# Performance work log

Hardware: AMD Instinct MI355X
Metric: run time of the kernel (lower is better)

Reference implementation:

```python
import jax, jax.numpy as jnp
import numpy as np

B, L, D_MODEL = 2, 2048, 1024
N_HEAD, D_K, D_V = 16, 64, 64


def setup_inputs() -> dict:
    key = jax.random.key(0)
    ks = jax.random.split(key, 11)
    s = lambda fan_in: 1.0 / np.sqrt(fan_in)
    return {
        "q": jax.random.normal(ks[0], (B, L, D_MODEL), dtype=jnp.float32),
        "k": jax.random.normal(ks[1], (B, L, D_MODEL), dtype=jnp.float32),
        "v": jax.random.normal(ks[2], (B, L, D_MODEL), dtype=jnp.float32),
        "Wq": jax.random.uniform(ks[3], (D_MODEL, N_HEAD * D_K), jnp.float32, -s(D_MODEL), s(D_MODEL)),
        "bq": jax.random.uniform(ks[4], (N_HEAD * D_K,), jnp.float32, -s(D_MODEL), s(D_MODEL)),
        "Wk": jax.random.uniform(ks[5], (D_MODEL, N_HEAD * D_K), jnp.float32, -s(D_MODEL), s(D_MODEL)),
        "bk": jax.random.uniform(ks[6], (N_HEAD * D_K,), jnp.float32, -s(D_MODEL), s(D_MODEL)),
        "Wv": jax.random.uniform(ks[7], (D_MODEL, N_HEAD * D_V), jnp.float32, -s(D_MODEL), s(D_MODEL)),
        "bv": jax.random.uniform(ks[8], (N_HEAD * D_V,), jnp.float32, -s(D_MODEL), s(D_MODEL)),
        "Wo": jax.random.uniform(ks[9], (N_HEAD * D_V, D_MODEL), jnp.float32, -s(N_HEAD * D_V), s(N_HEAD * D_V)),
        "bo": jax.random.uniform(ks[10], (D_MODEL,), jnp.float32, -s(N_HEAD * D_V), s(N_HEAD * D_V)),
    }


def reference(q, k, v, Wq, bq, Wk, bk, Wv, bv, Wo, bo):
    b, lq, _ = q.shape
    lk = k.shape[1]
    # QKV projections then split heads: [B, H, L, Dk]
    qh = (q @ Wq + bq).reshape(b, lq, N_HEAD, D_K).transpose(0, 2, 1, 3)
    kh = (k @ Wk + bk).reshape(b, lk, N_HEAD, D_K).transpose(0, 2, 1, 3)
    vh = (v @ Wv + bv).reshape(b, lk, N_HEAD, D_V).transpose(0, 2, 1, 3)
    # naive SDPA: materialize [B, H, Lq, Lk] scores, scale by sqrt(d_k)
    scores = jnp.einsum("bhqd,bhkd->bhqk", qh, kh) / jnp.sqrt(jnp.float32(D_K))
    attn = jax.nn.softmax(scores, axis=-1)
    out = jnp.einsum("bhqk,bhkd->bhqd", attn, vh)
    # merge heads and output projection (dropout = identity in eval)
    out = out.transpose(0, 2, 1, 3).reshape(b, lq, N_HEAD * D_V)
    out = out @ Wo + bo
    return out, attn
```

## Files before the change

kernel.cpp:

```cpp
#include <hip/hip_runtime.h>
#include <hip/hip_bf16.h>

typedef float f32x4 __attribute__((ext_vector_type(4)));
typedef short bf16x8 __attribute__((ext_vector_type(8)));

#define MFMA_BF16 __builtin_amdgcn_mfma_f32_16x16x32_bf16

static __device__ __forceinline__ unsigned short f2bf(float f) {
    __hip_bfloat16 h = __float2bfloat16(f);
    return __builtin_bit_cast(unsigned short, h);
}
static __device__ __forceinline__ unsigned int pack2(float a, float b) {
    return (unsigned int)f2bf(a) | ((unsigned int)f2bf(b) << 16);
}

static __device__ __forceinline__ void gl16(const unsigned short* g, unsigned short* l) {
    unsigned short* gg = const_cast<unsigned short*>(g);
    __builtin_amdgcn_global_load_lds(
        (__attribute__((address_space(1))) unsigned int*)gg,
        (__attribute__((address_space(3))) unsigned int*)l, 16, 0, 0);
}

__global__ __launch_bounds__(256) void conv_wT(
    const float* __restrict__ Wq, const float* __restrict__ Wk,
    const float* __restrict__ Wv, const float* __restrict__ Wo,
    unsigned short* __restrict__ WT)
{
    const int z = blockIdx.z;
    const float* W = (z == 0) ? Wq : (z == 1) ? Wk : (z == 2) ? Wv : Wo;
    unsigned short* Wt = WT + (size_t)z * 1048576;
    const int k0 = blockIdx.x * 64, n0 = blockIdx.y * 64;
    __shared__ float tl[64][68];
    const int t = threadIdx.x;
    const int r = t >> 2, cs = (t & 3) * 16;
#pragma unroll
    for (int j = 0; j < 4; j++)
        *(float4*)&tl[r][cs + j * 4] = *(const float4*)&W[(size_t)(k0 + r) * 1024 + n0 + cs + j * 4];
    __syncthreads();
    const int n = t & 63, kb = (t >> 6) * 16;
#pragma unroll
    for (int j = 0; j < 4; j++) {
        const int kk = kb + j * 4;
        uint2 o = { pack2(tl[kk][n], tl[kk + 1][n]), pack2(tl[kk + 2][n], tl[kk + 3][n]) };
        *(uint2*)&Wt[(size_t)(n0 + n) * 1024 + k0 + kk] = o;
    }
}

__global__ __launch_bounds__(256) void conv_bf16(
    const float* __restrict__ q, const float* __restrict__ k, const float* __restrict__ v,
    unsigned short* __restrict__ qkvb)
{
    const int z = blockIdx.y;
    const float* s = (z == 0) ? q : (z == 1) ? k : v;
    unsigned short* d = qkvb + (size_t)z * 4194304;
    const size_t i = ((size_t)blockIdx.x * 256 + threadIdx.x) * 8;
    float4 a = *(const float4*)&s[i], b = *(const float4*)&s[i + 4];
    uint4 o = { pack2(a.x, a.y), pack2(a.z, a.w), pack2(b.x, b.y), pack2(b.z, b.w) };
    *(uint4*)&d[i] = o;
}

static __device__ __forceinline__ void gemm_core(
    const unsigned short* __restrict__ A, const unsigned short* __restrict__ Bt,
    unsigned short* lA, unsigned short* lB, int m0, int n0, f32x4 (&acc)[4][4])
{
    const int t = threadIdx.x;
    const int w = t >> 6, lane = t & 63, lrow = lane & 15, lkg = lane >> 4;
    const int wr = w >> 1, wc = w & 1;
    const int srow = lane >> 2, sseg = (lane & 3) * 8;

    const unsigned short* Ab0 = &A[(size_t)(m0 + w * 32 + srow) * 1024 + sseg];
    const unsigned short* Ab1 = &A[(size_t)(m0 + w * 32 + 16 + srow) * 1024 + sseg];
    const unsigned short* Bb0 = &Bt[(size_t)(n0 + w * 32 + srow) * 1024 + sseg];
    const unsigned short* Bb1 = &Bt[(size_t)(n0 + w * 32 + 16 + srow) * 1024 + sseg];

#define GISSUE(tt, buf)                                     \
    do {                                                    \
        const int k0_ = (tt) * 32;                          \
        gl16(Ab0 + k0_, &lA[(buf) * 4096 + w * 1024]);      \
        gl16(Ab1 + k0_, &lA[(buf) * 4096 + w * 1024 + 512]);\
        gl16(Bb0 + k0_, &lB[(buf) * 4096 + w * 1024]);      \
        gl16(Bb1 + k0_, &lB[(buf) * 4096 + w * 1024 + 512]);\
    } while (0)

    GISSUE(0, 0);
    GISSUE(1, 1);
    __builtin_amdgcn_sched_barrier(0);

    int bcur = 0;
    for (int tt = 0; tt < 32; ++tt) {
        if (tt < 31) { asm volatile("s_waitcnt vmcnt(4)"); }
        else         { asm volatile("s_waitcnt vmcnt(0)"); }
        __builtin_amdgcn_s_barrier();
        __builtin_amdgcn_sched_barrier(0);
        if (tt + 2 < 32) {
            int bpre = bcur + 2; if (bpre >= 3) bpre -= 3;
            GISSUE(tt + 2, bpre);
        }
        __builtin_amdgcn_sched_barrier(0);

        const unsigned short* la = &lA[bcur * 4096];
        const unsigned short* lb = &lB[bcur * 4096];
        bf16x8 af[4], bfr[4];
#pragma unroll
        for (int mi = 0; mi < 4; mi++)
            af[mi] = *(const bf16x8*)&la[(wr * 64 + mi * 16 + lrow) * 32 + lkg * 8];
#pragma unroll
        for (int ni = 0; ni < 4; ni++)
            bfr[ni] = *(const bf16x8*)&lb[(wc * 64 + ni * 16 + lrow) * 32 + lkg * 8];
        __builtin_amdgcn_s_setprio(1);
#pragma unroll
        for (int mi = 0; mi < 4; mi++)
#pragma unroll
            for (int ni = 0; ni < 4; ni++)
                acc[mi][ni] = MFMA_BF16(af[mi], bfr[ni], acc[mi][ni], 0, 0, 0);
        __builtin_amdgcn_s_setprio(0);
        bcur = (bcur == 2) ? 0 : bcur + 1;
    }
#undef GISSUE
}

__global__ __launch_bounds__(256) void gemm_qkv(
    const unsigned short* __restrict__ qkvb, const unsigned short* __restrict__ WT,
    const float* __restrict__ bq, const float* __restrict__ bk, const float* __restrict__ bv,
    unsigned short* __restrict__ Qh, unsigned short* __restrict__ Kh, unsigned short* __restrict__ Vt)
{
    const int u0 = blockIdx.x;
    const int u = (u0 & 7) * 96 + (u0 >> 3);
    const int z = u >> 8, rm = u & 255;
    const int m0 = ((rm >> 3) & 31) * 128, n0 = (rm & 7) * 128;

    const unsigned short* A = qkvb + (size_t)z * 4194304;
    const unsigned short* Bt = WT + (size_t)z * 1048576;
    const float* bias = (z == 0) ? bq : (z == 1) ? bk : bv;

    __shared__ unsigned short lA[3 * 4096], lB[3 * 4096];
    f32x4 acc[4][4];
#pragma unroll
    for (int i = 0; i < 4; i++)
#pragma unroll
        for (int j = 0; j < 4; j++) acc[i][j] = (f32x4){0.f, 0.f, 0.f, 0.f};

    gemm_core(A, Bt, lA, lB, m0, n0, acc);

    const int t = threadIdx.x;
    const int w = t >> 6, lane = t & 63, lrow = lane & 15, lkg = lane >> 4;
    const int wr = w >> 1, wc = w & 1;

#pragma unroll
    for (int mi = 0; mi < 4; mi++) {
#pragma unroll
        for (int ni = 0; ni < 4; ni++) {
            const int gn = n0 + wc * 64 + ni * 16 + lrow;
            const float bb = bias[gn];
            const int hh = gn >> 6, dk = gn & 63;
            const int gm0 = m0 + wr * 64 + mi * 16 + lkg * 4;
            const int b2 = gm0 >> 11, ll = gm0 & 2047;
            if (z < 2) {
                unsigned short* C = (z == 0) ? Qh : Kh;
#pragma unroll
                for (int r = 0; r < 4; r++)
                    C[(size_t)((b2 * 16 + hh) * 2048 + ll + r) * 64 + dk] = f2bf(acc[mi][ni][r] + bb);
            } else {
                uint2 o = { pack2(acc[mi][ni][0] + bb, acc[mi][ni][1] + bb),
                            pack2(acc[mi][ni][2] + bb, acc[mi][ni][3] + bb) };
                *(uint2*)&Vt[(size_t)((b2 * 16 + hh) * 64 + dk) * 2048 + ll] = o;
            }
        }
    }
}

__global__ __launch_bounds__(256) void gemm_o(
    const unsigned short* __restrict__ Oh, const unsigned short* __restrict__ WoT,
    const float* __restrict__ bo, float* __restrict__ out)
{
    const int u0 = blockIdx.x;
    const int u = (u0 & 7) * 32 + (u0 >> 3);
    const int m0 = (u >> 3) * 128, n0 = (u & 7) * 128;

    __shared__ unsigned short lA[3 * 4096], lB[3 * 4096];
    f32x4 acc[4][4];
#pragma unroll
    for (int i = 0; i < 4; i++)
#pragma unroll
        for (int j = 0; j < 4; j++) acc[i][j] = (f32x4){0.f, 0.f, 0.f, 0.f};

    gemm_core(Oh, WoT, lA, lB, m0, n0, acc);

    const int t = threadIdx.x;
    const int w = t >> 6, lane = t & 63, lrow = lane & 15, lkg = lane >> 4;
    const int wr = w >> 1, wc = w & 1;

#pragma unroll
    for (int mi = 0; mi < 4; mi++) {
#pragma unroll
        for (int ni = 0; ni < 4; ni++) {
            const int gn = n0 + wc * 64 + ni * 16 + lrow;
            const float bb = bo[gn];
            const int gm0 = m0 + wr * 64 + mi * 16 + lkg * 4;
#pragma unroll
            for (int r = 0; r < 4; r++)
                out[(size_t)(gm0 + r) * 1024 + gn] = acc[mi][ni][r] + bb;
        }
    }
}

__global__ __launch_bounds__(256, 4) void attn_kernel(
    const unsigned short* __restrict__ Qh, const unsigned short* __restrict__ Kh,
    const unsigned short* __restrict__ Vt, float* __restrict__ attn,
    unsigned short* __restrict__ Oh)
{
    const int bid = blockIdx.x;
    const int swz = (bid & 7) * 128 + (bid >> 3);
    const int bh = swz >> 5;
    const int q0 = (swz & 31) * 64;
    const int b = bh >> 4, h = bh & 15;
    const int t = threadIdx.x;
    const int w = t >> 6, lane = t & 63, ql = lane & 15, kg = lane >> 4;

    __shared__ unsigned short regA[8192];
    __shared__ unsigned short kv[8192];

    const size_t kvbase = (size_t)bh * 2048 * 64;
    const float C = 0.18033688011112042f;

    const unsigned short* qptr = Qh + kvbase + (size_t)(q0 + w * 16 + ql) * 64 + kg * 8;
    const bf16x8 qf0 = *(const bf16x8*)(qptr);
    const bf16x8 qf1 = *(const bf16x8*)(qptr + 32);

    const unsigned short* Kbh = Kh + kvbase;
    const unsigned short* Vbh = Vt + kvbase;

    const int kr = w * 16 + (lane >> 3);
    const int kc = (lane & 7) ^ (kr & 7);
    const int r7 = ql & 7;

    f32x4 ls4 = (f32x4){0.f, 0.f, 0.f, 0.f};
    {
        gl16(Kbh + (size_t)kr * 64 + kc * 8, &regA[w * 1024]);
        gl16(Kbh + (size_t)(kr + 8) * 64 + kc * 8, &regA[w * 1024 + 512]);
        __syncthreads();
        for (int kt = 0; kt < 32; ++kt) {
            const int c = kt & 1;
            if (kt < 31) {
                const int k0n = (kt + 1) * 64;
                gl16(Kbh + (size_t)(k0n + kr) * 64 + kc * 8, &regA[(c ^ 1) * 4096 + w * 1024]);
                gl16(Kbh + (size_t)(k0n + kr + 8) * 64 + kc * 8, &regA[(c ^ 1) * 4096 + w * 1024 + 512]);
            } else {
                gl16(Kbh + (size_t)kr * 64 + kc * 8, &kv[w * 1024]);
                gl16(Kbh + (size_t)(kr + 8) * 64 + kc * 8, &kv[w * 1024 + 512]);
                gl16(Vbh + (size_t)kr * 2048 + kc * 8, &kv[4096 + w * 1024]);
                gl16(Vbh + (size_t)(kr + 8) * 2048 + kc * 8, &kv[4096 + w * 1024 + 512]);
            }
            const unsigned short* Kl = &regA[c * 4096];
            f32x4 sacc[4];
            __builtin_amdgcn_s_setprio(1);
#pragma unroll
            for (int ni = 0; ni < 4; ni++) {
                const int rb = (ni * 16 + ql) * 64;
                bf16x8 kf0 = *(const bf16x8*)&Kl[rb + ((kg ^ r7) * 8)];
                bf16x8 kf1 = *(const bf16x8*)&Kl[rb + (((4 + kg) ^ r7) * 8)];
                f32x4 s = (f32x4){0.f, 0.f, 0.f, 0.f};
                s = MFMA_BF16(kf0, qf0, s, 0, 0, 0);
                sacc[ni] = MFMA_BF16(kf1, qf1, s, 0, 0, 0);
            }
            __builtin_amdgcn_s_setprio(0);
#pragma unroll
            for (int ni = 0; ni < 4; ni++)
#pragma unroll
                for (int r = 0; r < 4; r++) ls4[r] += exp2f(sacc[ni][r] * C);
            __syncthreads();
        }
    }
    float lsum = ls4[0] + ls4[1] + ls4[2] + ls4[3];
    lsum += __shfl_xor(lsum, 16);
    lsum += __shfl_xor(lsum, 32);
    const float mlg = -log2f(lsum);

    f32x4 acco[4];
#pragma unroll
    for (int nv = 0; nv < 4; nv++) acco[nv] = (f32x4){0.f, 0.f, 0.f, 0.f};

    float* stgW = (float*)regA + w * 1024;
    const unsigned short* kvK = kv;
    const unsigned short* kvV = kv + 4096;
    float* abase = attn + ((size_t)bh * 2048 + q0 + w * 16) * 2048 + ql * 4;

    for (int kt = 0; kt < 32; ++kt) {
        const int k0 = kt * 64;

        f32x4 sacc[4];
        __builtin_amdgcn_s_setprio(1);
#pragma unroll
        for (int ni = 0; ni < 4; ni++) {
            const int rb = (ni * 16 + ql) * 64;
            bf16x8 kf0 = *(const bf16x8*)&kvK[rb + ((kg ^ r7) * 8)];
            bf16x8 kf1 = *(const bf16x8*)&kvK[rb + (((4 + kg) ^ r7) * 8)];
            f32x4 s = (f32x4){0.f, 0.f, 0.f, 0.f};
            s = MFMA_BF16(kf0, qf0, s, 0, 0, 0);
            sacc[ni] = MFMA_BF16(kf1, qf1, s, 0, 0, 0);
        }
        __builtin_amdgcn_s_setprio(0);

#pragma unroll
        for (int ni = 0; ni < 4; ni++) {
            f32x4 p;
#pragma unroll
            for (int r = 0; r < 4; r++) p[r] = exp2f(fmaf(sacc[ni][r], C, mlg));
            *(f32x4*)&stgW[ql * 64 + ni * 16 + kg * 4] = p;
        }

        __builtin_amdgcn_s_setprio(1);
#pragma unroll
        for (int s4 = 0; s4 < 2; s4++) {
            const float* ps = &stgW[ql * 64 + s4 * 32 + kg * 8];
            f32x4 pa = *(const f32x4*)ps;
            f32x4 pb = *(const f32x4*)(ps + 4);
            uint4 pw = { pack2(pa[0], pa[1]), pack2(pa[2], pa[3]),
                         pack2(pb[0], pb[1]), pack2(pb[2], pb[3]) };
            bf16x8 pf = __builtin_bit_cast(bf16x8, pw);
#pragma unroll
            for (int nv = 0; nv < 4; nv++) {
                const int cc = (s4 * 4 + kg) ^ r7;
                bf16x8 vf = *(const bf16x8*)&kvV[(nv * 16 + ql) * 64 + cc * 8];
                acco[nv] = MFMA_BF16(vf, pf, acco[nv], 0, 0, 0);
            }
        }
        __builtin_amdgcn_s_setprio(0);

        __builtin_amdgcn_s_barrier();
        __builtin_amdgcn_sched_barrier(0);

        if (kt < 31) {
            const int k0n = (kt + 1) * 64;
            gl16(Kbh + (size_t)(k0n + kr) * 64 + kc * 8, &kv[w * 1024]);
            gl16(Kbh + (size_t)(k0n + kr + 8) * 64 + kc * 8, &kv[w * 1024 + 512]);
            gl16(Vbh + (size_t)kr * 2048 + k0n + kc * 8, &kv[4096 + w * 1024]);
            gl16(Vbh + (size_t)(kr + 8) * 2048 + k0n + kc * 8, &kv[4096 + w * 1024 + 512]);
        }
        __builtin_amdgcn_sched_barrier(0);

#pragma unroll
        for (int i = 0; i < 4; i++) {
            const int row = i * 4 + kg;
            f32x4 vv = *(const f32x4*)&stgW[row * 64 + ql * 4];
            __builtin_nontemporal_store(vv, (f32x4*)&abase[(size_t)row * 2048 + k0]);
        }

        asm volatile("s_waitcnt vmcnt(4)");
        __builtin_amdgcn_s_barrier();
        __builtin_amdgcn_sched_barrier(0);
    }
    asm volatile("s_waitcnt vmcnt(0)");

    unsigned short* obase = Oh + ((size_t)(b * 2048 + q0 + w * 16 + ql)) * 1024 + h * 64 + kg * 4;
#pragma unroll
    for (int nv = 0; nv < 4; nv++) {
        uint2 o2 = { pack2(acco[nv][0], acco[nv][1]), pack2(acco[nv][2], acco[nv][3]) };
        *(uint2*)&obase[nv * 16] = o2;
    }
}

extern "C" void kernel_launch(void* const* d_in, const int* in_sizes, int n_in,
                              void* d_out, int out_size, void* d_ws, size_t ws_size,
                              hipStream_t stream) {
    const float* q  = (const float*)d_in[0];
    const float* k  = (const float*)d_in[1];
    const float* v  = (const float*)d_in[2];
    const float* Wq = (const float*)d_in[3];
    const float* bq = (const float*)d_in[4];
    const float* Wk = (const float*)d_in[5];
    const float* bk = (const float*)d_in[6];
    const float* Wv = (const float*)d_in[7];
    const float* bv = (const float*)d_in[8];
    const float* Wo = (const float*)d_in[9];
    const float* bo = (const float*)d_in[10];

    float* out  = (float*)d_out;
    float* attn = out + (size_t)2 * 2048 * 1024;

    const size_t HS = 4194304;
    unsigned short* qkvb = (unsigned short*)d_ws;
    unsigned short* WT   = qkvb + 3 * HS;
    unsigned short* Qh   = WT + 4 * 1048576;
    unsigned short* Kh   = Qh + HS;
    unsigned short* Vt   = Kh + HS;
    unsigned short* Oh   = Vt + HS;

    conv_wT  <<<dim3(16, 16, 4), 256, 0, stream>>>(Wq, Wk, Wv, Wo, WT);
    conv_bf16<<<dim3(2048, 3),  256, 0, stream>>>(q, k, v, qkvb);
    gemm_qkv <<<dim3(768), 256, 0, stream>>>(qkvb, WT, bq, bk, bv, Qh, Kh, Vt);
    attn_kernel<<<dim3(1024), 256, 0, stream>>>(Qh, Kh, Vt, attn, Oh);
    gemm_o   <<<dim3(256), 256, 0, stream>>>(Oh, WT + 3 * 1048576, bo, out);
}
```

Measured before the change: 242.2 us.

## Vectorize GEMM epilogue stores via swapped MFMA operands and LDS-staged V transpose

```diff
diff --git a/kernel.cpp b/kernel.cpp
--- a/kernel.cpp
+++ b/kernel.cpp
@@ -37,12 +37,16 @@
     for (int j = 0; j < 4; j++)
         *(float4*)&tl[r][cs + j * 4] = *(const float4*)&W[(size_t)(k0 + r) * 1024 + n0 + cs + j * 4];
     __syncthreads();
-    const int n = t & 63, kb = (t >> 6) * 16;
-#pragma unroll
-    for (int j = 0; j < 4; j++) {
-        const int kk = kb + j * 4;
-        uint2 o = { pack2(tl[kk][n], tl[kk + 1][n]), pack2(tl[kk + 2][n], tl[kk + 3][n]) };
-        *(uint2*)&Wt[(size_t)(n0 + n) * 1024 + k0 + kk] = o;
+#pragma unroll
+    for (int pass = 0; pass < 2; pass++) {
+        const int n = (t >> 3) + pass * 32;
+        const int ks = (t & 7) * 8;
+        uint4 o;
+        unsigned int* op = (unsigned int*)&o;
+#pragma unroll
+        for (int j = 0; j < 4; j++)
+            op[j] = pack2(tl[ks + 2 * j][n], tl[ks + 2 * j + 1][n]);
+        *(uint4*)&Wt[(size_t)(n0 + n) * 1024 + k0 + ks] = o;
     }
 }
 
@@ -59,6 +63,7 @@
     *(uint4*)&d[i] = o;
 }
 
+template <bool SWAP>
 static __device__ __forceinline__ void gemm_core(
     const unsigned short* __restrict__ A, const unsigned short* __restrict__ Bt,
     unsigned short* lA, unsigned short* lB, int m0, int n0, f32x4 (&acc)[4][4])
@@ -111,27 +116,30 @@
 #pragma unroll
         for (int mi = 0; mi < 4; mi++)
 #pragma unroll
-            for (int ni = 0; ni < 4; ni++)
-                acc[mi][ni] = MFMA_BF16(af[mi], bfr[ni], acc[mi][ni], 0, 0, 0);
+            for (int ni = 0; ni < 4; ni++) {
+                if (SWAP) acc[mi][ni] = MFMA_BF16(bfr[ni], af[mi], acc[mi][ni], 0, 0, 0);
+                else      acc[mi][ni] = MFMA_BF16(af[mi], bfr[ni], acc[mi][ni], 0, 0, 0);
+            }
         __builtin_amdgcn_s_setprio(0);
         bcur = (bcur == 2) ? 0 : bcur + 1;
     }
 #undef GISSUE
 }
 
-__global__ __launch_bounds__(256) void gemm_qkv(
+__global__ __launch_bounds__(256) void gemm_qk(
     const unsigned short* __restrict__ qkvb, const unsigned short* __restrict__ WT,
-    const float* __restrict__ bq, const float* __restrict__ bk, const float* __restrict__ bv,
-    unsigned short* __restrict__ Qh, unsigned short* __restrict__ Kh, unsigned short* __restrict__ Vt)
+    const float* __restrict__ bq, const float* __restrict__ bk,
+    unsigned short* __restrict__ Qh, unsigned short* __restrict__ Kh)
 {
     const int u0 = blockIdx.x;
-    const int u = (u0 & 7) * 96 + (u0 >> 3);
+    const int u = (u0 & 7) * 64 + (u0 >> 3);
     const int z = u >> 8, rm = u & 255;
-    const int m0 = ((rm >> 3) & 31) * 128, n0 = (rm & 7) * 128;
+    const int m0 = (rm >> 3) * 128, n0 = (rm & 7) * 128;
 
     const unsigned short* A = qkvb + (size_t)z * 4194304;
     const unsigned short* Bt = WT + (size_t)z * 1048576;
-    const float* bias = (z == 0) ? bq : (z == 1) ? bk : bv;
+    const float* bias = (z == 0) ? bq : bk;
+    unsigned short* C = (z == 0) ? Qh : Kh;
 
     __shared__ unsigned short lA[3 * 4096], lB[3 * 4096];
     f32x4 acc[4][4];
@@ -140,7 +148,7 @@
 #pragma unroll
         for (int j = 0; j < 4; j++) acc[i][j] = (f32x4){0.f, 0.f, 0.f, 0.f};
 
-    gemm_core(A, Bt, lA, lB, m0, n0, acc);
+    gemm_core<true>(A, Bt, lA, lB, m0, n0, acc);
 
     const int t = threadIdx.x;
     const int w = t >> 6, lane = t & 63, lrow = lane & 15, lkg = lane >> 4;
@@ -148,24 +156,72 @@
 
 #pragma unroll
     for (int mi = 0; mi < 4; mi++) {
+        const int m = m0 + wr * 64 + mi * 16 + lrow;
+        const int b2 = m >> 11, ll = m & 2047;
 #pragma unroll
         for (int ni = 0; ni < 4; ni++) {
-            const int gn = n0 + wc * 64 + ni * 16 + lrow;
-            const float bb = bias[gn];
-            const int hh = gn >> 6, dk = gn & 63;
-            const int gm0 = m0 + wr * 64 + mi * 16 + lkg * 4;
-            const int b2 = gm0 >> 11, ll = gm0 & 2047;
-            if (z < 2) {
-                unsigned short* C = (z == 0) ? Qh : Kh;
-#pragma unroll
-                for (int r = 0; r < 4; r++)
-                    C[(size_t)((b2 * 16 + hh) * 2048 + ll + r) * 64 + dk] = f2bf(acc[mi][ni][r] + bb);
-            } else {
-                uint2 o = { pack2(acc[mi][ni][0] + bb, acc[mi][ni][1] + bb),
-                            pack2(acc[mi][ni][2] + bb, acc[mi][ni][3] + bb) };
-                *(uint2*)&Vt[(size_t)((b2 * 16 + hh) * 64 + dk) * 2048 + ll] = o;
-            }
-        }
+            const int gnb = n0 + wc * 64 + ni * 16 + lkg * 4;
+            const f32x4 bb4 = *(const f32x4*)&bias[gnb];
+            const int hh = gnb >> 6, dk = gnb & 63;
+            uint2 o = { pack2(acc[mi][ni][0] + bb4[0], acc[mi][ni][1] + bb4[1]),
+                        pack2(acc[mi][ni][2] + bb4[2], acc[mi][ni][3] + bb4[3]) };
+            *(uint2*)&C[(size_t)((b2 * 16 + hh) * 2048 + ll) * 64 + dk] = o;
+        }
+    }
+}
+
+__global__ __launch_bounds__(256) void gemm_v(
+    const unsigned short* __restrict__ qkvb, const unsigned short* __restrict__ WT,
+    const float* __restrict__ bv, unsigned short* __restrict__ Vt)
+{
+    const int u0 = blockIdx.x;
+    const int u = (u0 & 7) * 32 + (u0 >> 3);
+    const int m0 = (u >> 3) * 128, n0 = (u & 7) * 128;
+
+    const unsigned short* A = qkvb + (size_t)2 * 4194304;
+    const unsigned short* Bt = WT + (size_t)2 * 1048576;
+
+    __shared__ unsigned short pool[3 * 4096 * 2];
+    unsigned short* lA = pool;
+    unsigned short* lB = pool + 3 * 4096;
+
+    f32x4 acc[4][4];
+#pragma unroll
+    for (int i = 0; i < 4; i++)
+#pragma unroll
+        for (int j = 0; j < 4; j++) acc[i][j] = (f32x4){0.f, 0.f, 0.f, 0.f};
+
+    gemm_core<false>(A, Bt, lA, lB, m0, n0, acc);
+    __syncthreads();
+
+    const int t = threadIdx.x;
+    const int w = t >> 6, lane = t & 63, lrow = lane & 15, lkg = lane >> 4;
+    const int wr = w >> 1, wc = w & 1;
+
+    unsigned short* vt = pool;
+#pragma unroll
+    for (int mi = 0; mi < 4; mi++) {
+#pragma unroll
+        for (int ni = 0; ni < 4; ni++) {
+            const int gnl = wc * 64 + ni * 16 + lrow;
+            const float bb = bv[n0 + gnl];
+            const int ll = wr * 64 + mi * 16 + lkg * 4;
+            uint2 o = { pack2(acc[mi][ni][0] + bb, acc[mi][ni][1] + bb),
+                        pack2(acc[mi][ni][2] + bb, acc[mi][ni][3] + bb) };
+            *(uint2*)&vt[gnl * 136 + ll] = o;
+        }
+    }
+    __syncthreads();
+
+    const int b2 = m0 >> 11;
+    const int mb = m0 & 2047;
+#pragma unroll
+    for (int p = 0; p < 8; p++) {
+        const int gnl = (t >> 4) + p * 16;
+        const int l16 = t & 15;
+        const int gn = n0 + gnl, hh = gn >> 6, dk = gn & 63;
+        uint4 v4 = *(const uint4*)&vt[gnl * 136 + l16 * 8];
+        *(uint4*)&Vt[(size_t)((b2 * 16 + hh) * 64 + dk) * 2048 + mb + l16 * 8] = v4;
     }
 }
 
@@ -184,7 +240,7 @@
 #pragma unroll
         for (int j = 0; j < 4; j++) acc[i][j] = (f32x4){0.f, 0.f, 0.f, 0.f};
 
-    gemm_core(Oh, WoT, lA, lB, m0, n0, acc);
+    gemm_core<true>(Oh, WoT, lA, lB, m0, n0, acc);
 
     const int t = threadIdx.x;
     const int w = t >> 6, lane = t & 63, lrow = lane & 15, lkg = lane >> 4;
@@ -192,14 +248,13 @@
 
 #pragma unroll
     for (int mi = 0; mi < 4; mi++) {
+        const int m = m0 + wr * 64 + mi * 16 + lrow;
 #pragma unroll
         for (int ni = 0; ni < 4; ni++) {
-            const int gn = n0 + wc * 64 + ni * 16 + lrow;
-            const float bb = bo[gn];
-            const int gm0 = m0 + wr * 64 + mi * 16 + lkg * 4;
-#pragma unroll
-            for (int r = 0; r < 4; r++)
-                out[(size_t)(gm0 + r) * 1024 + gn] = acc[mi][ni][r] + bb;
+            const int gnb = n0 + wc * 64 + ni * 16 + lkg * 4;
+            const f32x4 bb4 = *(const f32x4*)&bo[gnb];
+            f32x4 o = acc[mi][ni] + bb4;
+            *(f32x4*)&out[(size_t)m * 1024 + gnb] = o;
         }
     }
 }
@@ -388,7 +443,8 @@
 
     conv_wT  <<<dim3(16, 16, 4), 256, 0, stream>>>(Wq, Wk, Wv, Wo, WT);
     conv_bf16<<<dim3(2048, 3),  256, 0, stream>>>(q, k, v, qkvb);
-    gemm_qkv <<<dim3(768), 256, 0, stream>>>(qkvb, WT, bq, bk, bv, Qh, Kh, Vt);
+    gemm_qk  <<<dim3(512), 256, 0, stream>>>(qkvb, WT, bq, bk, Qh, Kh);
+    gemm_v   <<<dim3(256), 256, 0, stream>>>(qkvb, WT, bv, Vt);
     attn_kernel<<<dim3(1024), 256, 0, stream>>>(Qh, Kh, Vt, attn, Oh);
     gemm_o   <<<dim3(256), 256, 0, stream>>>(Oh, WT + 3 * 1048576, bo, out);
 }
```

Measured after the change: 249.4 us. 1.03x slower.
